# Performance work log

Hardware: AMD Instinct MI355X
Metric: run time of the kernel (lower is better)

Reference implementation:

```python
import jax, jax.numpy as jnp
import numpy as np

NEG_SLOPE = 0.2  # PyG GATConv default negative_slope
N_NODES = 40000
N_EDGES = 640000
IN_DIM = 128
SAT_DIM = 64
HID = 128
OUT_DIM = 54


def gat_conv(x, edge_index, W, a_src, a_dst, bias):
    """PyG GATConv with heads=1, concat=True, add_self_loops=True."""
    n = x.shape[0]
    loops = jnp.arange(n, dtype=edge_index.dtype)
    src = jnp.concatenate([edge_index[0], loops])  # message sources j
    dst = jnp.concatenate([edge_index[1], loops])  # message targets i
    h = x @ W.T                                    # [N, C]
    alpha_s = h @ a_src                            # [N]
    alpha_d = h @ a_dst                            # [N]
    e = jax.nn.leaky_relu(alpha_s[src] + alpha_d[dst], NEG_SLOPE)  # [E]
    # segment softmax over incoming edges of each dst node (self-loops guarantee non-empty segments)
    m = jax.ops.segment_max(e, dst, num_segments=n)
    e = jnp.exp(e - m[dst])
    denom = jax.ops.segment_sum(e, dst, num_segments=n)
    alpha = e / (denom[dst] + 1e-16)
    out = jax.ops.segment_sum(alpha[:, None] * h[src], dst, num_segments=n)
    return out + bias


def setup_inputs() -> dict:
    key = jax.random.key(0)
    ks = jax.random.split(key, 16)
    s = lambda d: 1.0 / np.sqrt(d)
    inp = {
        "x": jax.random.normal(ks[0], (N_NODES, IN_DIM), jnp.float32),
        "edge_index": jax.random.randint(ks[1], (2, N_EDGES), 0, N_NODES, jnp.int32),
        "sat_W": jax.random.normal(ks[2], (HID, SAT_DIM), jnp.float32) * s(SAT_DIM),
        "sat_b": jnp.zeros((HID,), jnp.float32),
        "neigh_W": jax.random.normal(ks[3], (HID, IN_DIM - SAT_DIM), jnp.float32) * s(IN_DIM - SAT_DIM),
        "neigh_b": jnp.zeros((HID,), jnp.float32),
        "conv1_W": jax.random.normal(ks[4], (HID, HID), jnp.float32) * s(HID),
        "conv1_asrc": jax.random.normal(ks[5], (HID,), jnp.float32) * s(HID),
        "conv1_adst": jax.random.normal(ks[6], (HID,), jnp.float32) * s(HID),
        "conv1_b": jnp.zeros((HID,), jnp.float32),
        "conv2_W": jax.random.normal(ks[7], (HID, HID), jnp.float32) * s(HID),
        "conv2_asrc": jax.random.normal(ks[8], (HID,), jnp.float32) * s(HID),
        "conv2_adst": jax.random.normal(ks[9], (HID,), jnp.float32) * s(HID),
        "conv2_b": jnp.zeros((HID,), jnp.float32),
        "fc1_W": jax.random.normal(ks[10], (HID, HID), jnp.float32) * s(HID),
        "fc1_b": jnp.zeros((HID,), jnp.float32),
        "fc2_W": jax.random.normal(ks[11], (OUT_DIM, HID), jnp.float32) * s(HID),
        "fc2_b": jnp.zeros((OUT_DIM,), jnp.float32),
    }
    return inp


def reference(x, edge_index, sat_W, sat_b, neigh_W, neigh_b,
              conv1_W, conv1_asrc, conv1_adst, conv1_b,
              conv2_W, conv2_asrc, conv2_adst, conv2_b,
              fc1_W, fc1_b, fc2_W, fc2_b):
    sat = jax.nn.relu(x[:, :SAT_DIM] @ sat_W.T + sat_b)
    nei = jax.nn.relu(x[:, SAT_DIM:] @ neigh_W.T + neigh_b)
    h = sat + 0.5 * nei
    h = jax.nn.relu(gat_conv(h, edge_index, conv1_W, conv1_asrc, conv1_adst, conv1_b))
    h = jax.nn.relu(gat_conv(h, edge_index, conv2_W, conv2_asrc, conv2_adst, conv2_b))
    h = jax.nn.relu(h @ fc1_W.T + fc1_b)
    return h @ fc2_W.T + fc2_b
```

## Files before the change

### kernel.cpp

```cpp
#include <hip/hip_runtime.h>


#define N_NODES 40000
#define N_EDGES 640000
#define DIM     128

typedef unsigned short u16;
typedef __attribute__((ext_vector_type(8))) short bf16x8;
typedef __attribute__((ext_vector_type(4))) float f32x4;

__device__ __forceinline__ u16 f2bf(float v) {
    unsigned u = __float_as_uint(v);
    u += 0x7FFFu + ((u >> 16) & 1u);
    return (u16)(u >> 16);
}
__device__ __forceinline__ float bf2f(u16 h) { return __uint_as_float(((unsigned)h) << 16); }
__device__ __forceinline__ float rdlane_f(float v, int l) {
    return __uint_as_float(__builtin_amdgcn_readlane(__float_as_uint(v), l));
}

__device__ __forceinline__ int hswz(int row, int col) {
    return row * 128 + ((((col >> 2) ^ (row & 7))) << 2) + (col & 3);
}
__device__ __forceinline__ float4 hread4(const float* hbuf, int row, int k) {
    int b = (k >> 2) ^ (row & 7);
    return *(const float4*)&hbuf[row * 128 + (b << 2)];
}
__device__ __forceinline__ void split8(const float* vv, bf16x8& hi, bf16x8& lo) {
#pragma unroll
    for (int i = 0; i < 8; ++i) {
        u16 h = f2bf(vv[i]);
        hi[i] = (short)h;
        lo[i] = (short)f2bf(vv[i] - bf2f(h));
    }
}

__global__ __launch_bounds__(256) void k_wcvt(
    const float* __restrict__ satW, const float* __restrict__ neiW,
    const float* __restrict__ c1W, const float* __restrict__ c2W,
    const float* __restrict__ f1W, const float* __restrict__ f2W,
    u16* __restrict__ wa, int* __restrict__ deg, int* __restrict__ counter) {
    int gid = (blockIdx.y * gridDim.x + blockIdx.x) * 256 + threadIdx.x;
    if (gid < N_NODES) deg[gid] = 1;
    if (gid == 0) *counter = 0;

    int m = blockIdx.y;
    const float* src; int C, K, Cp; int offH, offL;
    switch (m) {
        case 0: src = satW; C = 128; K = 64;  Cp = 128; offH = 0;      offL = 8192;   break;
        case 1: src = neiW; C = 128; K = 64;  Cp = 128; offH = 16384;  offL = 24576;  break;
        case 2: src = c1W;  C = 128; K = 128; Cp = 128; offH = 32768;  offL = 49152;  break;
        case 3: src = c2W;  C = 128; K = 128; Cp = 128; offH = 65536;  offL = 81920;  break;
        case 4: src = f1W;  C = 128; K = 128; Cp = 128; offH = 98304;  offL = 114688; break;
        default:src = f2W;  C = 54;  K = 128; Cp = 64;  offH = 131072; offL = 139264; break;
    }
    int e = blockIdx.x * 256 + threadIdx.x;
    if (e >= Cp * K) return;
    int c = e / K, k = e - c * K;
    float v = (c < C) ? src[c * K + k] : 0.f;
    u16 h = f2bf(v);
    wa[offH + e] = h;
    wa[offL + e] = f2bf(v - bf2f(h));
}

__global__ void k_deg_count(const int* __restrict__ dst, int* __restrict__ deg) {
    int t = blockIdx.x * 256 + threadIdx.x;
    if (t < N_EDGES) atomicAdd(&deg[dst[t]], 1);
}
__global__ void k_assign(const int* __restrict__ deg, int* __restrict__ counter,
                         int* __restrict__ start, int* __restrict__ cursor,
                         int* __restrict__ csr_src) {
    int i = blockIdx.x * 256 + threadIdx.x;
    if (i >= N_NODES) return;
    int d = deg[i];
    int s = atomicAdd(counter, d);
    start[i] = s;
    csr_src[s] = i;
    cursor[i] = s + 1;
}
__global__ void k_fill_edges(const int* __restrict__ src, const int* __restrict__ dst,
                             int* __restrict__ cursor, int* __restrict__ csr_src) {
    int t = blockIdx.x * 256 + threadIdx.x;
    if (t < N_EDGES) {
        int p = atomicAdd(&cursor[dst[t]], 1);
        csr_src[p] = src[t];
    }
}

template<int CT>
__device__ __forceinline__ void stage_W(u16* Ws, const u16* __restrict__ Wh,
                                        const u16* __restrict__ Wl, int kc, int tid) {
    for (int idx = tid; idx < CT * 2 * 2 * 64; idx += 256) {
        int l = idx & 63;
        int q = idx >> 6;
        int hilo = q & 1;
        int ks = (q >> 1) & 1;
        int ct = q >> 2;
        int c = ct * 16 + (l & 15);
        int k = kc * 64 + ks * 32 + (l >> 4) * 8;
        const u16* Wp = hilo ? Wl : Wh;
        *reinterpret_cast<bf16x8*>(&Ws[idx * 8]) =
            *reinterpret_cast<const bf16x8*>(Wp + (size_t)c * 128 + k);
    }
}

#define MFMA3(ACC, AH, AL, BH, BL)                                             \
    ACC = __builtin_amdgcn_mfma_f32_16x16x32_bf16(AH, BH, ACC, 0, 0, 0);       \
    ACC = __builtin_amdgcn_mfma_f32_16x16x32_bf16(AH, BL, ACC, 0, 0, 0);       \
    ACC = __builtin_amdgcn_mfma_f32_16x16x32_bf16(AL, BH, ACC, 0, 0, 0);

__device__ __forceinline__ void alpha_epi(const f32x4* acc, int lane, int r0,
                                          const float* __restrict__ a_src,
                                          const float* __restrict__ a_dst,
                                          float* __restrict__ as_, float* __restrict__ ad_) {
    float ps[4] = {0, 0, 0, 0}, pd[4] = {0, 0, 0, 0};
#pragma unroll
    for (int ct = 0; ct < 8; ++ct) {
        float asv = a_src[ct * 16 + (lane & 15)];
        float adv = a_dst[ct * 16 + (lane & 15)];
#pragma unroll
        for (int r = 0; r < 4; ++r) {
            ps[r] = fmaf(acc[ct][r], asv, ps[r]);
            pd[r] = fmaf(acc[ct][r], adv, pd[r]);
        }
    }
#pragma unroll
    for (int off = 1; off < 16; off <<= 1) {
#pragma unroll
        for (int r = 0; r < 4; ++r) {
            ps[r] += __shfl_xor(ps[r], off);
            pd[r] += __shfl_xor(pd[r], off);
        }
    }
    if ((lane & 15) == 0) {
#pragma unroll
        for (int r = 0; r < 4; ++r) {
            int row = r0 + (lane >> 4) * 4 + r;
            as_[row] = ps[r];
            ad_[row] = pd[r];
        }
    }
}

__global__ __launch_bounds__(256) void k_enc_conv1(
    const float* __restrict__ x,
    const u16* __restrict__ sH, const u16* __restrict__ sL,
    const u16* __restrict__ nH, const u16* __restrict__ nL,
    const float* __restrict__ satb, const float* __restrict__ neib,
    const u16* __restrict__ Wh, const u16* __restrict__ Wl,
    const float* __restrict__ a_src, const float* __restrict__ a_dst,
    u16* __restrict__ outG, float* __restrict__ as_, float* __restrict__ ad_)
{
    __shared__ u16 Wbuf[16384];
    float* hbuf = (float*)Wbuf;
    const int tid = threadIdx.x, lane = tid & 63, wv = tid >> 6;
    const int r0 = blockIdx.x * 64 + wv * 16;
    const int arow = r0 + (lane & 15);
    const int kb = (lane >> 4) * 8;

    bf16x8 axh[4], axl[4];
#pragma unroll
    for (int s = 0; s < 4; ++s) {
        const float* p = x + (size_t)arow * 128 + s * 32 + kb;
        float4 a = *(const float4*)p;
        float4 b = *(const float4*)(p + 4);
        float vv[8] = {a.x, a.y, a.z, a.w, b.x, b.y, b.z, b.w};
        split8(vv, axh[s], axl[s]);
    }

    f32x4 accS[8], accN[8];
#pragma unroll
    for (int ct = 0; ct < 8; ++ct) { accS[ct] = (f32x4){0,0,0,0}; accN[ct] = (f32x4){0,0,0,0}; }

#pragma unroll
    for (int mat = 0; mat < 2; ++mat) {
        if (mat) __syncthreads();
        const u16* WH = mat ? nH : sH;
        const u16* WL = mat ? nL : sL;
        for (int idx = tid; idx < 2048; idx += 256) {
            int l = idx & 63;
            int q = idx >> 6;
            int hilo = q & 1;
            int ks = (q >> 1) & 1;
            int ct = q >> 2;
            int c = ct * 16 + (l & 15);
            int k = ks * 32 + (l >> 4) * 8;
            const u16* Wp = hilo ? WL : WH;
            *reinterpret_cast<bf16x8*>(&Wbuf[idx * 8]) =
                *reinterpret_cast<const bf16x8*>(Wp + (size_t)c * 64 + k);
        }
        __syncthreads();
#pragma unroll
        for (int ct = 0; ct < 8; ++ct) {
#pragma unroll
            for (int ks = 0; ks < 2; ++ks) {
                int s = mat * 2 + ks;
                int base = (ct * 2 + ks) * 1024;
                bf16x8 bh = *reinterpret_cast<const bf16x8*>(&Wbuf[base + lane * 8]);
                bf16x8 bl = *reinterpret_cast<const bf16x8*>(&Wbuf[base + 512 + lane * 8]);
                f32x4* ac = mat ? &accN[ct] : &accS[ct];
                MFMA3((*ac), axh[s], axl[s], bh, bl);
            }
        }
    }
    __syncthreads();

#pragma unroll
    for (int ct = 0; ct < 8; ++ct) {
        int c = ct * 16 + (lane & 15);
        float bs = satb[c], bn = neib[c];
#pragma unroll
        for (int r = 0; r < 4; ++r) {
            int rl = wv * 16 + (lane >> 4) * 4 + r;
            float v = fmaxf(accS[ct][r] + bs, 0.f) + 0.5f * fmaxf(accN[ct][r] + bn, 0.f);
            hbuf[hswz(rl, c)] = v;
        }
    }
    __syncthreads();

    bf16x8 ah[4], al[4];
    const int ar = wv * 16 + (lane & 15);
#pragma unroll
    for (int s = 0; s < 4; ++s) {
        int k0 = s * 32 + kb;
        float4 a = hread4(hbuf, ar, k0);
        float4 b = hread4(hbuf, ar, k0 + 4);
        float vv[8] = {a.x, a.y, a.z, a.w, b.x, b.y, b.z, b.w};
        split8(vv, ah[s], al[s]);
    }
    __syncthreads();

    f32x4 acc[8];
#pragma unroll
    for (int ct = 0; ct < 8; ++ct) acc[ct] = (f32x4){0, 0, 0, 0};
#pragma unroll
    for (int kc = 0; kc < 2; ++kc) {
        if (kc) __syncthreads();
        stage_W<8>(Wbuf, Wh, Wl, kc, tid);
        __syncthreads();
#pragma unroll
        for (int ct = 0; ct < 8; ++ct) {
#pragma unroll
            for (int ks = 0; ks < 2; ++ks) {
                int s = kc * 2 + ks;
                int base = (ct * 2 + ks) * 1024;
                bf16x8 bh = *reinterpret_cast<const bf16x8*>(&Wbuf[base + lane * 8]);
                bf16x8 bl = *reinterpret_cast<const bf16x8*>(&Wbuf[base + 512 + lane * 8]);
                MFMA3(acc[ct], ah[s], al[s], bh, bl);
            }
        }
    }

    alpha_epi(acc, lane, r0, a_src, a_dst, as_, ad_);

#pragma unroll
    for (int ct = 0; ct < 8; ++ct) {
        int c = ct * 16 + (lane & 15);
#pragma unroll
        for (int r = 0; r < 4; ++r) {
            int row = r0 + (lane >> 4) * 4 + r;
            outG[(size_t)row * 128 + c] = f2bf(acc[ct][r]);
        }
    }
}

__global__ __launch_bounds__(256) void k_conv_gemm(
    const u16* __restrict__ Ah, const u16* __restrict__ Al,
    const u16* __restrict__ Wh, const u16* __restrict__ Wl,
    const float* __restrict__ a_src, const float* __restrict__ a_dst,
    u16* __restrict__ outG, float* __restrict__ as_, float* __restrict__ ad_)
{
    __shared__ u16 Wbuf[16384];
    const int tid = threadIdx.x, lane = tid & 63, wv = tid >> 6;
    const int r0 = blockIdx.x * 64 + wv * 16;
    const int arow = r0 + (lane & 15);
    const int kb = (lane >> 4) * 8;

    bf16x8 ah[4], al[4];
#pragma unroll
    for (int s = 0; s < 4; ++s) {
        ah[s] = *reinterpret_cast<const bf16x8*>(Ah + (size_t)arow * 128 + s * 32 + kb);
        al[s] = *reinterpret_cast<const bf16x8*>(Al + (size_t)arow * 128 + s * 32 + kb);
    }

    f32x4 acc[8];
#pragma unroll
    for (int ct = 0; ct < 8; ++ct) acc[ct] = (f32x4){0, 0, 0, 0};
#pragma unroll
    for (int kc = 0; kc < 2; ++kc) {
        if (kc) __syncthreads();
        stage_W<8>(Wbuf, Wh, Wl, kc, tid);
        __syncthreads();
#pragma unroll
        for (int ct = 0; ct < 8; ++ct) {
#pragma unroll
            for (int ks = 0; ks < 2; ++ks) {
                int s = kc * 2 + ks;
                int base = (ct * 2 + ks) * 1024;
                bf16x8 bh = *reinterpret_cast<const bf16x8*>(&Wbuf[base + lane * 8]);
                bf16x8 bl = *reinterpret_cast<const bf16x8*>(&Wbuf[base + 512 + lane * 8]);
                MFMA3(acc[ct], ah[s], al[s], bh, bl);
            }
        }
    }

    alpha_epi(acc, lane, r0, a_src, a_dst, as_, ad_);

#pragma unroll
    for (int ct = 0; ct < 8; ++ct) {
        int c = ct * 16 + (lane & 15);
#pragma unroll
        for (int r = 0; r < 4; ++r) {
            int row = r0 + (lane >> 4) * 4 + r;
            outG[(size_t)row * 128 + c] = f2bf(acc[ct][r]);
        }
    }
}

__global__ __launch_bounds__(256) void k_fc12(
    const u16* __restrict__ Ah, const u16* __restrict__ Al,
    const u16* __restrict__ W1h, const u16* __restrict__ W1l, const float* __restrict__ b1,
    const u16* __restrict__ W2h, const u16* __restrict__ W2l, const float* __restrict__ b2,
    float* __restrict__ out)
{
    __shared__ u16 Wbuf[16384];
    float* hbuf = (float*)Wbuf;
    const int tid = threadIdx.x, lane = tid & 63, wv = tid >> 6;
    const int r0 = blockIdx.x * 64 + wv * 16;
    const int arow = r0 + (lane & 15);
    const int kb = (lane >> 4) * 8;

    bf16x8 ah[4], al[4];
#pragma unroll
    for (int s = 0; s < 4; ++s) {
        ah[s] = *reinterpret_cast<const bf16x8*>(Ah + (size_t)arow * 128 + s * 32 + kb);
        al[s] = *reinterpret_cast<const bf16x8*>(Al + (size_t)arow * 128 + s * 32 + kb);
    }

    f32x4 acc[8];
#pragma unroll
    for (int ct = 0; ct < 8; ++ct) acc[ct] = (f32x4){0, 0, 0, 0};
#pragma unroll
    for (int kc = 0; kc < 2; ++kc) {
        if (kc) __syncthreads();
        stage_W<8>(Wbuf, W1h, W1l, kc, tid);
        __syncthreads();
#pragma unroll
        for (int ct = 0; ct < 8; ++ct) {
#pragma unroll
            for (int ks = 0; ks < 2; ++ks) {
                int s = kc * 2 + ks;
                int base = (ct * 2 + ks) * 1024;
                bf16x8 bh = *reinterpret_cast<const bf16x8*>(&Wbuf[base + lane * 8]);
                bf16x8 bl = *reinterpret_cast<const bf16x8*>(&Wbuf[base + 512 + lane * 8]);
                MFMA3(acc[ct], ah[s], al[s], bh, bl);
            }
        }
    }
    __syncthreads();

#pragma unroll
    for (int ct = 0; ct < 8; ++ct) {
        int c = ct * 16 + (lane & 15);
        float bv = b1[c];
#pragma unroll
        for (int r = 0; r < 4; ++r) {
            int rl = wv * 16 + (lane >> 4) * 4 + r;
            hbuf[hswz(rl, c)] = fmaxf(acc[ct][r] + bv, 0.f);
        }
    }
    __syncthreads();

    bf16x8 a2h[4], a2l[4];
    const int ar = wv * 16 + (lane & 15);
#pragma unroll
    for (int s = 0; s < 4; ++s) {
        int k0 = s * 32 + kb;
        float4 a = hread4(hbuf, ar, k0);
        float4 b = hread4(hbuf, ar, k0 + 4);
        float vv[8] = {a.x, a.y, a.z, a.w, b.x, b.y, b.z, b.w};
        split8(vv, a2h[s], a2l[s]);
    }
    __syncthreads();

    f32x4 acc2[4];
#pragma unroll
    for (int ct = 0; ct < 4; ++ct) acc2[ct] = (f32x4){0, 0, 0, 0};
#pragma unroll
    for (int kc = 0; kc < 2; ++kc) {
        if (kc) __syncthreads();
        stage_W<4>(Wbuf, W2h, W2l, kc, tid);
        __syncthreads();
#pragma unroll
        for (int ct = 0; ct < 4; ++ct) {
#pragma unroll
            for (int ks = 0; ks < 2; ++ks) {
                int s = kc * 2 + ks;
                int base = (ct * 2 + ks) * 1024;
                bf16x8 bh = *reinterpret_cast<const bf16x8*>(&Wbuf[base + lane * 8]);
                bf16x8 bl = *reinterpret_cast<const bf16x8*>(&Wbuf[base + 512 + lane * 8]);
                MFMA3(acc2[ct], a2h[s], a2l[s], bh, bl);
            }
        }
    }

#pragma unroll
    for (int ct = 0; ct < 4; ++ct) {
        int c = ct * 16 + (lane & 15);
#pragma unroll
        for (int r = 0; r < 4; ++r) {
            int row = r0 + (lane >> 4) * 4 + r;
            if (c < 54) out[(size_t)row * 54 + c] = acc2[ct][r] + b2[c];
        }
    }
}

#define DO_PAIRS(NP, TB)                                                      \
    {                                                                         \
        float pw[NP]; const ushort4* hp[NP];                                  \
        _Pragma("unroll")                                                     \
        for (int q = 0; q < NP; ++q) {                                        \
            int e0 = (TB) + 2 * q;                                            \
            float plo = rdlane_f(p, e0), phi = rdlane_f(p, e0 + 1);           \
            int jlo = __builtin_amdgcn_readlane(jj, e0);                      \
            int jhi = __builtin_amdgcn_readlane(jj, e0 + 1);                  \
            pw[q] = hodd ? phi : plo;                                         \
            int j = hodd ? jhi : jlo;                                         \
            hp[q] = (const ushort4*)&hg[(size_t)j * 128 + 4 * l32];           \
        }                                                                     \
        ushort4 hv[NP];                                                       \
        _Pragma("unroll") for (int q = 0; q < NP; ++q) hv[q] = *hp[q];        \
        _Pragma("unroll") for (int q = 0; q < NP; ++q) {                      \
            acc.x = fmaf(pw[q], bf2f(hv[q].x), acc.x);                        \
            acc.y = fmaf(pw[q], bf2f(hv[q].y), acc.y);                        \
            acc.z = fmaf(pw[q], bf2f(hv[q].z), acc.z);                        \
            acc.w = fmaf(pw[q], bf2f(hv[q].w), acc.w);                        \
        }                                                                     \
    }

__global__ __launch_bounds__(256) void k_aggregate(
    const u16* __restrict__ hg, const float* __restrict__ as_,
    const float* __restrict__ ad_, const int* __restrict__ start,
    const int* __restrict__ deg, const int* __restrict__ csr_src,
    const float* __restrict__ bias, u16* __restrict__ outH, u16* __restrict__ outL)
{
    int wid = (blockIdx.x * 256 + threadIdx.x) >> 6;
    int lane = threadIdx.x & 63;
    if (wid >= N_NODES) return;

    const int s0 = start[wid];
    const int s1 = s0 + deg[wid];
    const float adi = ad_[wid];
    const int l32 = lane & 31;
    const bool hodd = lane >= 32;

    float4 acc = make_float4(0.f, 0.f, 0.f, 0.f);
    float ssum = 0.f;
    for (int base = s0; base < s1; base += 64) {
        int k = base + lane;
        int cnt = min(64, s1 - base);
        int jj = 0;
        float p = 0.f;
        if (k < s1) {
            jj = csr_src[k];
            float e = as_[jj] + adi;
            e = (e > 0.f) ? e : 0.2f * e;
            p = __expf(e);
            ssum += p;
        }
        int t = 0;
        for (; t + 16 <= cnt; t += 16) DO_PAIRS(8, t)
        if (t + 8 <= cnt) { DO_PAIRS(4, t) t += 8; }
        if (t + 4 <= cnt) { DO_PAIRS(2, t) t += 4; }
        for (; t < cnt; t += 2) DO_PAIRS(1, t)
    }
#pragma unroll
    for (int off = 32; off; off >>= 1) ssum += __shfl_xor(ssum, off);
    acc.x += __shfl_xor(acc.x, 32);
    acc.y += __shfl_xor(acc.y, 32);
    acc.z += __shfl_xor(acc.z, 32);
    acc.w += __shfl_xor(acc.w, 32);
    float inv = 1.f / (ssum + 1e-16f);

    if (!hodd) {
        float4 bv = *(const float4*)&bias[4 * l32];
        float o0 = fmaxf(fmaf(acc.x, inv, bv.x), 0.f);
        float o1 = fmaxf(fmaf(acc.y, inv, bv.y), 0.f);
        float o2 = fmaxf(fmaf(acc.z, inv, bv.z), 0.f);
        float o3 = fmaxf(fmaf(acc.w, inv, bv.w), 0.f);
        u16 h0 = f2bf(o0), h1 = f2bf(o1), h2 = f2bf(o2), h3 = f2bf(o3);
        ushort4 hvv = make_ushort4(h0, h1, h2, h3);
        ushort4 lvv = make_ushort4(f2bf(o0 - bf2f(h0)), f2bf(o1 - bf2f(h1)),
                                   f2bf(o2 - bf2f(h2)), f2bf(o3 - bf2f(h3)));
        *(ushort4*)&outH[(size_t)wid * 128 + 4 * l32] = hvv;
        *(ushort4*)&outL[(size_t)wid * 128 + 4 * l32] = lvv;
    }
}

extern "C" void kernel_launch(void* const* d_in, const int* in_sizes, int n_in,
                              void* d_out, int out_size, void* d_ws, size_t ws_size,
                              hipStream_t stream) {
    (void)in_sizes; (void)n_in; (void)out_size; (void)ws_size;

    const float* x       = (const float*)d_in[0];
    const int*   ei      = (const int*)d_in[1];
    const float* sat_W   = (const float*)d_in[2];
    const float* sat_b   = (const float*)d_in[3];
    const float* neigh_W = (const float*)d_in[4];
    const float* neigh_b = (const float*)d_in[5];
    const float* c1_W    = (const float*)d_in[6];
    const float* c1_as   = (const float*)d_in[7];
    const float* c1_ad   = (const float*)d_in[8];
    const float* c1_b    = (const float*)d_in[9];
    const float* c2_W    = (const float*)d_in[10];
    const float* c2_as   = (const float*)d_in[11];
    const float* c2_ad   = (const float*)d_in[12];
    const float* c2_b    = (const float*)d_in[13];
    const float* fc1_W   = (const float*)d_in[14];
    const float* fc1_b   = (const float*)d_in[15];
    const float* fc2_W   = (const float*)d_in[16];
    const float* fc2_b   = (const float*)d_in[17];

    const int* e_src = ei;
    const int* e_dst = ei + N_EDGES;

    char* w = (char*)d_ws;
    u16*   hG     = (u16*)  (w);
    u16*   hH     = (u16*)  (w + 10240000);
    u16*   hL     = (u16*)  (w + 20480000);
    float* as_    = (float*)(w + 30720000);
    float* ad_    = (float*)(w + 30880000);
    int*   deg    = (int*)  (w + 31040000);
    int*   start  = (int*)  (w + 31200000);
    int*   cursor = (int*)  (w + 31360000);
    int*   counter= (int*)  (w + 31520000);
    int*   csr    = (int*)  (w + 31520256);
    u16*   wa     = (u16*)  (w + 34240256);

    u16 *satH = wa,          *satL = wa + 8192;
    u16 *neiH = wa + 16384,  *neiL = wa + 24576;
    u16 *c1H  = wa + 32768,  *c1L  = wa + 49152;
    u16 *c2H  = wa + 65536,  *c2L  = wa + 81920;
    u16 *f1H  = wa + 98304,  *f1L  = wa + 114688;
    u16 *f2H  = wa + 131072, *f2L  = wa + 139264;

    dim3 b(256);
    k_wcvt<<<dim3(64, 6), b, 0, stream>>>(sat_W, neigh_W, c1_W, c2_W, fc1_W, fc2_W,
                                          wa, deg, counter);
    k_deg_count <<<2500, b, 0, stream>>>(e_dst, deg);
    k_assign    <<<157,  b, 0, stream>>>(deg, counter, start, cursor, csr);
    k_fill_edges<<<2500, b, 0, stream>>>(e_src, e_dst, cursor, csr);

    k_enc_conv1<<<625, b, 0, stream>>>(x, satH, satL, neiH, neiL, sat_b, neigh_b,
                                       c1H, c1L, c1_as, c1_ad, hG, as_, ad_);
    k_aggregate<<<10000, b, 0, stream>>>(hG, as_, ad_, start, deg, csr, c1_b, hH, hL);

    k_conv_gemm<<<625, b, 0, stream>>>(hH, hL, c2H, c2L, c2_as, c2_ad, hG, as_, ad_);
    k_aggregate<<<10000, b, 0, stream>>>(hG, as_, ad_, start, deg, csr, c2_b, hH, hL);

    k_fc12<<<625, b, 0, stream>>>(hH, hL, f1H, f1L, fc1_b, f2H, f2L, fc2_b,
                                  (float*)d_out);
}
```

Baseline: 202.4 us.

## Split GEMM columns across two waves per row tile with 512-thread blocks

The three dense GEMM kernels now launch 512 threads per block. Each 16-row tile is handled by two waves, each computing half of the output columns, which halves per-wave accumulators and MFMA work. The attention-logit dot products are now partial per column half and are combined through a small shared-memory reduction with an extra barrier. This is meant to raise parallelism and latency hiding on 625-block grids, at the cost of duplicated A-operand loads and bf16 splitting in both waves, plus extra synchronisation.

```diff
diff --git a/kernel.cpp b/kernel.cpp
--- a/kernel.cpp
+++ b/kernel.cpp
@@ -34,6 +34,11 @@
         lo[i] = (short)f2bf(vv[i] - bf2f(h));
     }
 }
+
+#define MFMA3(ACC, AH, AL, BH, BL)                                             \
+    ACC = __builtin_amdgcn_mfma_f32_16x16x32_bf16(AH, BH, ACC, 0, 0, 0);       \
+    ACC = __builtin_amdgcn_mfma_f32_16x16x32_bf16(AH, BL, ACC, 0, 0, 0);       \
+    ACC = __builtin_amdgcn_mfma_f32_16x16x32_bf16(AL, BH, ACC, 0, 0, 0);
 
 __global__ __launch_bounds__(256) void k_wcvt(
     const float* __restrict__ satW, const float* __restrict__ neiW,
@@ -87,10 +92,9 @@
     }
 }
 
-template<int CT>
-__device__ __forceinline__ void stage_W(u16* Ws, const u16* __restrict__ Wh,
-                                        const u16* __restrict__ Wl, int kc, int tid) {
-    for (int idx = tid; idx < CT * 2 * 2 * 64; idx += 256) {
+__device__ __forceinline__ void stage_W128(u16* Ws, const u16* __restrict__ Wh,
+                                           const u16* __restrict__ Wl, int kc, int tid) {
+    for (int idx = tid; idx < 2048; idx += 512) {
         int l = idx & 63;
         int q = idx >> 6;
         int hilo = q & 1;
@@ -103,21 +107,31 @@
             *reinterpret_cast<const bf16x8*>(Wp + (size_t)c * 128 + k);
     }
 }
-
-#define MFMA3(ACC, AH, AL, BH, BL)                                             \
-    ACC = __builtin_amdgcn_mfma_f32_16x16x32_bf16(AH, BH, ACC, 0, 0, 0);       \
-    ACC = __builtin_amdgcn_mfma_f32_16x16x32_bf16(AH, BL, ACC, 0, 0, 0);       \
-    ACC = __builtin_amdgcn_mfma_f32_16x16x32_bf16(AL, BH, ACC, 0, 0, 0);
-
-__device__ __forceinline__ void alpha_epi(const f32x4* acc, int lane, int r0,
-                                          const float* __restrict__ a_src,
-                                          const float* __restrict__ a_dst,
-                                          float* __restrict__ as_, float* __restrict__ ad_) {
+__device__ __forceinline__ void stage_W64(u16* Ws, const u16* __restrict__ Wh,
+                                          const u16* __restrict__ Wl, int tid) {
+    for (int idx = tid; idx < 2048; idx += 512) {
+        int l = idx & 63;
+        int q = idx >> 6;
+        int hilo = q & 1;
+        int ks = (q >> 1) & 1;
+        int ct = q >> 2;
+        int c = ct * 16 + (l & 15);
+        int k = ks * 32 + (l >> 4) * 8;
+        const u16* Wp = hilo ? Wl : Wh;
+        *reinterpret_cast<bf16x8*>(&Ws[idx * 8]) =
+            *reinterpret_cast<const bf16x8*>(Wp + (size_t)c * 64 + k);
+    }
+}
+
+__device__ __forceinline__ void alpha_colsplit(
+    const f32x4* acc, int lane, int colgrp, int rowgrp, int tid, int brow0,
+    const float* __restrict__ a_src, const float* __restrict__ a_dst,
+    float (*redbuf)[2][64], float* __restrict__ as_, float* __restrict__ ad_) {
     float ps[4] = {0, 0, 0, 0}, pd[4] = {0, 0, 0, 0};
 #pragma unroll
-    for (int ct = 0; ct < 8; ++ct) {
-        float asv = a_src[ct * 16 + (lane & 15)];
-        float adv = a_dst[ct * 16 + (lane & 15)];
+    for (int ct = 0; ct < 4; ++ct) {
+        int c = colgrp * 64 + ct * 16 + (lane & 15);
+        float asv = a_src[c], adv = a_dst[c];
 #pragma unroll
         for (int r = 0; r < 4; ++r) {
             ps[r] = fmaf(acc[ct][r], asv, ps[r]);
@@ -135,14 +149,19 @@
     if ((lane & 15) == 0) {
 #pragma unroll
         for (int r = 0; r < 4; ++r) {
-            int row = r0 + (lane >> 4) * 4 + r;
-            as_[row] = ps[r];
-            ad_[row] = pd[r];
-        }
-    }
-}
-
-__global__ __launch_bounds__(256) void k_enc_conv1(
+            int rl = rowgrp * 16 + (lane >> 4) * 4 + r;
+            redbuf[0][colgrp][rl] = ps[r];
+            redbuf[1][colgrp][rl] = pd[r];
+        }
+    }
+    __syncthreads();
+    if (tid < 64) {
+        as_[brow0 + tid] = redbuf[0][0][tid] + redbuf[0][1][tid];
+        ad_[brow0 + tid] = redbuf[1][0][tid] + redbuf[1][1][tid];
+    }
+}
+
+__global__ __launch_bounds__(512) void k_enc_conv1(
     const float* __restrict__ x,
     const u16* __restrict__ sH, const u16* __restrict__ sL,
     const u16* __restrict__ nH, const u16* __restrict__ nL,
@@ -152,9 +171,12 @@
     u16* __restrict__ outG, float* __restrict__ as_, float* __restrict__ ad_)
 {
     __shared__ u16 Wbuf[16384];
+    __shared__ float redbuf[2][2][64];
     float* hbuf = (float*)Wbuf;
     const int tid = threadIdx.x, lane = tid & 63, wv = tid >> 6;
-    const int r0 = blockIdx.x * 64 + wv * 16;
+    const int rowgrp = wv >> 1, colgrp = wv & 1;
+    const int brow0 = blockIdx.x * 64;
+    const int r0 = brow0 + rowgrp * 16;
     const int arow = r0 + (lane & 15);
     const int kb = (lane >> 4) * 8;
 
@@ -168,34 +190,22 @@
         split8(vv, axh[s], axl[s]);
     }
 
-    f32x4 accS[8], accN[8];
-#pragma unroll
-    for (int ct = 0; ct < 8; ++ct) { accS[ct] = (f32x4){0,0,0,0}; accN[ct] = (f32x4){0,0,0,0}; }
+    f32x4 accS[4], accN[4];
+#pragma unroll
+    for (int ct = 0; ct < 4; ++ct) { accS[ct] = (f32x4){0,0,0,0}; accN[ct] = (f32x4){0,0,0,0}; }
 
 #pragma unroll
     for (int mat = 0; mat < 2; ++mat) {
         if (mat) __syncthreads();
-        const u16* WH = mat ? nH : sH;
-        const u16* WL = mat ? nL : sL;
-        for (int idx = tid; idx < 2048; idx += 256) {
-            int l = idx & 63;
-            int q = idx >> 6;
-            int hilo = q & 1;
-            int ks = (q >> 1) & 1;
-            int ct = q >> 2;
-            int c = ct * 16 + (l & 15);
-            int k = ks * 32 + (l >> 4) * 8;
-            const u16* Wp = hilo ? WL : WH;
-            *reinterpret_cast<bf16x8*>(&Wbuf[idx * 8]) =
-                *reinterpret_cast<const bf16x8*>(Wp + (size_t)c * 64 + k);
-        }
+        stage_W64(Wbuf, mat ? nH : sH, mat ? nL : sL, tid);
         __syncthreads();
 #pragma unroll
-        for (int ct = 0; ct < 8; ++ct) {
+        for (int ct = 0; ct < 4; ++ct) {
+            int ctG = colgrp * 4 + ct;
 #pragma unroll
             for (int ks = 0; ks < 2; ++ks) {
                 int s = mat * 2 + ks;
-                int base = (ct * 2 + ks) * 1024;
+                int base = (ctG * 2 + ks) * 1024;
                 bf16x8 bh = *reinterpret_cast<const bf16x8*>(&Wbuf[base + lane * 8]);
                 bf16x8 bl = *reinterpret_cast<const bf16x8*>(&Wbuf[base + 512 + lane * 8]);
                 f32x4* ac = mat ? &accN[ct] : &accS[ct];
@@ -206,12 +216,12 @@
     __syncthreads();
 
 #pragma unroll
-    for (int ct = 0; ct < 8; ++ct) {
-        int c = ct * 16 + (lane & 15);
+    for (int ct = 0; ct < 4; ++ct) {
+        int c = colgrp * 64 + ct * 16 + (lane & 15);
         float bs = satb[c], bn = neib[c];
 #pragma unroll
         for (int r = 0; r < 4; ++r) {
-            int rl = wv * 16 + (lane >> 4) * 4 + r;
+            int rl = rowgrp * 16 + (lane >> 4) * 4 + r;
             float v = fmaxf(accS[ct][r] + bs, 0.f) + 0.5f * fmaxf(accN[ct][r] + bn, 0.f);
             hbuf[hswz(rl, c)] = v;
         }
@@ -219,7 +229,7 @@
     __syncthreads();
 
     bf16x8 ah[4], al[4];
-    const int ar = wv * 16 + (lane & 15);
+    const int ar = rowgrp * 16 + (lane & 15);
 #pragma unroll
     for (int s = 0; s < 4; ++s) {
         int k0 = s * 32 + kb;
@@ -230,20 +240,21 @@
     }
     __syncthreads();
 
-    f32x4 acc[8];
-#pragma unroll
-    for (int ct = 0; ct < 8; ++ct) acc[ct] = (f32x4){0, 0, 0, 0};
+    f32x4 acc[4];
+#pragma unroll
+    for (int ct = 0; ct < 4; ++ct) acc[ct] = (f32x4){0, 0, 0, 0};
 #pragma unroll
     for (int kc = 0; kc < 2; ++kc) {
         if (kc) __syncthreads();
-        stage_W<8>(Wbuf, Wh, Wl, kc, tid);
+        stage_W128(Wbuf, Wh, Wl, kc, tid);
         __syncthreads();
 #pragma unroll
-        for (int ct = 0; ct < 8; ++ct) {
+        for (int ct = 0; ct < 4; ++ct) {
+            int ctG = colgrp * 4 + ct;
 #pragma unroll
             for (int ks = 0; ks < 2; ++ks) {
                 int s = kc * 2 + ks;
-                int base = (ct * 2 + ks) * 1024;
+                int base = (ctG * 2 + ks) * 1024;
                 bf16x8 bh = *reinterpret_cast<const bf16x8*>(&Wbuf[base + lane * 8]);
                 bf16x8 bl = *reinterpret_cast<const bf16x8*>(&Wbuf[base + 512 + lane * 8]);
                 MFMA3(acc[ct], ah[s], al[s], bh, bl);
@@ -251,11 +262,11 @@
         }
     }
 
-    alpha_epi(acc, lane, r0, a_src, a_dst, as_, ad_);
-
-#pragma unroll
-    for (int ct = 0; ct < 8; ++ct) {
-        int c = ct * 16 + (lane & 15);
+    alpha_colsplit(acc, lane, colgrp, rowgrp, tid, brow0, a_src, a_dst, redbuf, as_, ad_);
+
+#pragma unroll
+    for (int ct = 0; ct < 4; ++ct) {
+        int c = colgrp * 64 + ct * 16 + (lane & 15);
 #pragma unroll
         for (int r = 0; r < 4; ++r) {
             int row = r0 + (lane >> 4) * 4 + r;
@@ -264,15 +275,18 @@
     }
 }
 
-__global__ __launch_bounds__(256) void k_conv_gemm(
+__global__ __launch_bounds__(512) void k_conv_gemm(
     const u16* __restrict__ Ah, const u16* __restrict__ Al,
     const u16* __restrict__ Wh, const u16* __restrict__ Wl,
     const float* __restrict__ a_src, const float* __restrict__ a_dst,
     u16* __restrict__ outG, float* __restrict__ as_, float* __restrict__ ad_)
 {
     __shared__ u16 Wbuf[16384];
+    __shared__ float redbuf[2][2][64];
     const int tid = threadIdx.x, lane = tid & 63, wv = tid >> 6;
-    const int r0 = blockIdx.x * 64 + wv * 16;
+    const int rowgrp = wv >> 1, colgrp = wv & 1;
+    const int brow0 = blockIdx.x * 64;
+    const int r0 = brow0 + rowgrp * 16;
     const int arow = r0 + (lane & 15);
     const int kb = (lane >> 4) * 8;
 
@@ -283,20 +297,21 @@
         al[s] = *reinterpret_cast<const bf16x8*>(Al + (size_t)arow * 128 + s * 32 + kb);
     }
 
-    f32x4 acc[8];
-#pragma unroll
-    for (int ct = 0; ct < 8; ++ct) acc[ct] = (f32x4){0, 0, 0, 0};
+    f32x4 acc[4];
+#pragma unroll
+    for (int ct = 0; ct < 4; ++ct) acc[ct] = (f32x4){0, 0, 0, 0};
 #pragma unroll
     for (int kc = 0; kc < 2; ++kc) {
         if (kc) __syncthreads();
-        stage_W<8>(Wbuf, Wh, Wl, kc, tid);
+        stage_W128(Wbuf, Wh, Wl, kc, tid);
         __syncthreads();
 #pragma unroll
-        for (int ct = 0; ct < 8; ++ct) {
+        for (int ct = 0; ct < 4; ++ct) {
+            int ctG = colgrp * 4 + ct;
 #pragma unroll
             for (int ks = 0; ks < 2; ++ks) {
                 int s = kc * 2 + ks;
-                int base = (ct * 2 + ks) * 1024;
+                int base = (ctG * 2 + ks) * 1024;
                 bf16x8 bh = *reinterpret_cast<const bf16x8*>(&Wbuf[base + lane * 8]);
                 bf16x8 bl = *reinterpret_cast<const bf16x8*>(&Wbuf[base + 512 + lane * 8]);
                 MFMA3(acc[ct], ah[s], al[s], bh, bl);
@@ -304,11 +319,11 @@
         }
     }
 
-    alpha_epi(acc, lane, r0, a_src, a_dst, as_, ad_);
-
-#pragma unroll
-    for (int ct = 0; ct < 8; ++ct) {
-        int c = ct * 16 + (lane & 15);
+    alpha_colsplit(acc, lane, colgrp, rowgrp, tid, brow0, a_src, a_dst, redbuf, as_, ad_);
+
+#pragma unroll
+    for (int ct = 0; ct < 4; ++ct) {
+        int c = colgrp * 64 + ct * 16 + (lane & 15);
 #pragma unroll
         for (int r = 0; r < 4; ++r) {
             int row = r0 + (lane >> 4) * 4 + r;
@@ -317,7 +332,7 @@
     }
 }
 
-__global__ __launch_bounds__(256) void k_fc12(
+__global__ __launch_bounds__(512) void k_fc12(
     const u16* __restrict__ Ah, const u16* __restrict__ Al,
     const u16* __restrict__ W1h, const u16* __restrict__ W1l, const float* __restrict__ b1,
     const u16* __restrict__ W2h, const u16* __restrict__ W2l, const float* __restrict__ b2,
@@ -326,7 +341,8 @@
     __shared__ u16 Wbuf[16384];
     float* hbuf = (float*)Wbuf;
     const int tid = threadIdx.x, lane = tid & 63, wv = tid >> 6;
-    const int r0 = blockIdx.x * 64 + wv * 16;
+    const int rowgrp = wv >> 1, colgrp = wv & 1;
+    const int r0 = blockIdx.x * 64 + rowgrp * 16;
     const int arow = r0 + (lane & 15);
     const int kb = (lane >> 4) * 8;
 
@@ -337,20 +353,21 @@
         al[s] = *reinterpret_cast<const bf16x8*>(Al + (size_t)arow * 128 + s * 32 + kb);
     }
 
-    f32x4 acc[8];
-#pragma unroll
-    for (int ct = 0; ct < 8; ++ct) acc[ct] = (f32x4){0, 0, 0, 0};
+    f32x4 acc[4];
+#pragma unroll
+    for (int ct = 0; ct < 4; ++ct) acc[ct] = (f32x4){0, 0, 0, 0};
 #pragma unroll
     for (int kc = 0; kc < 2; ++kc) {
         if (kc) __syncthreads();
-        stage_W<8>(Wbuf, W1h, W1l, kc, tid);
+        stage_W128(Wbuf, W1h, W1l, kc, tid);
         __syncthreads();
 #pragma unroll
-        for (int ct = 0; ct < 8; ++ct) {
+        for (int ct = 0; ct < 4; ++ct) {
+            int ctG = colgrp * 4 + ct;
 #pragma unroll
             for (int ks = 0; ks < 2; ++ks) {
                 int s = kc * 2 + ks;
-                int base = (ct * 2 + ks) * 1024;
+                int base = (ctG * 2 + ks) * 1024;
                 bf16x8 bh = *reinterpret_cast<const bf16x8*>(&Wbuf[base + lane * 8]);
                 bf16x8 bl = *reinterpret_cast<const bf16x8*>(&Wbuf[base + 512 + lane * 8]);
                 MFMA3(acc[ct], ah[s], al[s], bh, bl);
@@ -360,19 +377,19 @@
     __syncthreads();
 
 #pragma unroll
-    for (int ct = 0; ct < 8; ++ct) {
-        int c = ct * 16 + (lane & 15);
+    for (int ct = 0; ct < 4; ++ct) {
+        int c = colgrp * 64 + ct * 16 + (lane & 15);
         float bv = b1[c];
 #pragma unroll
         for (int r = 0; r < 4; ++r) {
-            int rl = wv * 16 + (lane >> 4) * 4 + r;
+            int rl = rowgrp * 16 + (lane >> 4) * 4 + r;
             hbuf[hswz(rl, c)] = fmaxf(acc[ct][r] + bv, 0.f);
         }
     }
     __syncthreads();
 
     bf16x8 a2h[4], a2l[4];
-    const int ar = wv * 16 + (lane & 15);
+    const int ar = rowgrp * 16 + (lane & 15);
 #pragma unroll
     for (int s = 0; s < 4; ++s) {
         int k0 = s * 32 + kb;
@@ -383,20 +400,32 @@
     }
     __syncthreads();
 
-    f32x4 acc2[4];
-#pragma unroll
-    for (int ct = 0; ct < 4; ++ct) acc2[ct] = (f32x4){0, 0, 0, 0};
+    f32x4 acc2[2];
+#pragma unroll
+    for (int ct = 0; ct < 2; ++ct) acc2[ct] = (f32x4){0, 0, 0, 0};
 #pragma unroll
     for (int kc = 0; kc < 2; ++kc) {
         if (kc) __syncthreads();
-        stage_W<4>(Wbuf, W2h, W2l, kc, tid);
+        for (int idx = tid; idx < 1024; idx += 512) {
+            int l = idx & 63;
+            int q = idx >> 6;
+            int hilo = q & 1;
+            int ks = (q >> 1) & 1;
+            int ct = q >> 2;
+            int c = ct * 16 + (l & 15);
+            int k = kc * 64 + ks * 32 + (l >> 4) * 8;
+            const u16* Wp = hilo ? W2l : W2h;
+            *reinterpret_cast<bf16x8*>(&Wbuf[idx * 8]) =
+                *reinterpret_cast<const bf16x8*>(Wp + (size_t)c * 128 + k);
+        }
         __syncthreads();
 #pragma unroll
-        for (int ct = 0; ct < 4; ++ct) {
+        for (int ct = 0; ct < 2; ++ct) {
+            int ctG = colgrp * 2 + ct;
 #pragma unroll
             for (int ks = 0; ks < 2; ++ks) {
                 int s = kc * 2 + ks;
-                int base = (ct * 2 + ks) * 1024;
+                int base = (ctG * 2 + ks) * 1024;
                 bf16x8 bh = *reinterpret_cast<const bf16x8*>(&Wbuf[base + lane * 8]);
                 bf16x8 bl = *reinterpret_cast<const bf16x8*>(&Wbuf[base + 512 + lane * 8]);
                 MFMA3(acc2[ct], a2h[s], a2l[s], bh, bl);
@@ -405,8 +434,8 @@
     }
 
 #pragma unroll
-    for (int ct = 0; ct < 4; ++ct) {
-        int c = ct * 16 + (lane & 15);
+    for (int ct = 0; ct < 2; ++ct) {
+        int c = colgrp * 32 + ct * 16 + (lane & 15);
 #pragma unroll
         for (int r = 0; r < 4; ++r) {
             int row = r0 + (lane >> 4) * 4 + r;
@@ -545,19 +574,20 @@
     u16 *f2H  = wa + 131072, *f2L  = wa + 139264;
 
     dim3 b(256);
+    dim3 b512(512);
     k_wcvt<<<dim3(64, 6), b, 0, stream>>>(sat_W, neigh_W, c1_W, c2_W, fc1_W, fc2_W,
                                           wa, deg, counter);
     k_deg_count <<<2500, b, 0, stream>>>(e_dst, deg);
     k_assign    <<<157,  b, 0, stream>>>(deg, counter, start, cursor, csr);
     k_fill_edges<<<2500, b, 0, stream>>>(e_src, e_dst, cursor, csr);
 
-    k_enc_conv1<<<625, b, 0, stream>>>(x, satH, satL, neiH, neiL, sat_b, neigh_b,
-                                       c1H, c1L, c1_as, c1_ad, hG, as_, ad_);
+    k_enc_conv1<<<625, b512, 0, stream>>>(x, satH, satL, neiH, neiL, sat_b, neigh_b,
+                                          c1H, c1L, c1_as, c1_ad, hG, as_, ad_);
     k_aggregate<<<10000, b, 0, stream>>>(hG, as_, ad_, start, deg, csr, c1_b, hH, hL);
 
-    k_conv_gemm<<<625, b, 0, stream>>>(hH, hL, c2H, c2L, c2_as, c2_ad, hG, as_, ad_);
+    k_conv_gemm<<<625, b512, 0, stream>>>(hH, hL, c2H, c2L, c2_as, c2_ad, hG, as_, ad_);
     k_aggregate<<<10000, b, 0, stream>>>(hG, as_, ad_, start, deg, csr, c2_b, hH, hL);
 
-    k_fc12<<<625, b, 0, stream>>>(hH, hL, f1H, f1L, fc1_b, f2H, f2L, fc2_b,
-                                  (float*)d_out);
-}
+    k_fc12<<<625, b512, 0, stream>>>(hH, hL, f1H, f1L, fc1_b, f2H, f2L, fc2_b,
+                                     (float*)d_out);
+}
```

Result: slower. 209.8 us (+3.7%).
